# Kernel tuning notes

Hardware: AMD Instinct MI355X
Metric: run time of the kernel (lower is better)

The kernel has to match this reference:

```python
import jax, jax.numpy as jnp
import numpy as np

B, H, W, C = 4, 48, 48, 256
NQ = 8
NH = 8
FFN = 1024


def _dwconv(x, w, b):
    # x: (b,h,w,c); w: (kh,kw,1,c) depthwise; b: (c,)
    p = w.shape[0] // 2
    y = jax.lax.conv_general_dilated(
        x, w, (1, 1), [(p, p), (p, p)],
        dimension_numbers=('NHWC', 'HWIO', 'NHWC'),
        feature_group_count=x.shape[-1])
    return y + b


def _ln(x, g, b, eps=1e-6):
    m = jnp.mean(x, -1, keepdims=True)
    v = jnp.mean((x - m) ** 2, -1, keepdims=True)
    return (x - m) * jax.lax.rsqrt(v + eps) * g + b


def setup_inputs() -> dict:
    key = jax.random.key(0)
    ks = jax.random.split(key, 16)
    s = lambda k, sh, sc=0.02: jax.random.normal(k, sh, jnp.float32) * sc
    return dict(
        x=jax.random.normal(ks[0], (B, H, W, C), jnp.float32),
        queries=jax.random.normal(ks[1], (B, NQ, C), jnp.float32),
        epoch=10,
        pos_w=s(ks[2], (3, 3, 1, C)), pos_b=jnp.zeros((C,), jnp.float32),
        ln1_g=jnp.ones((C,), jnp.float32), ln1_b=jnp.zeros((C,), jnp.float32),
        q_w=s(ks[3], (C, C)), q_b=jnp.zeros((C,), jnp.float32),
        k_w=s(ks[4], (C, C)), k_b=jnp.zeros((C,), jnp.float32),
        v_w=s(ks[5], (C, C)), v_b=jnp.zeros((C,), jnp.float32),
        lepe_w=s(ks[6], (5, 5, 1, C)), lepe_b=jnp.zeros((C,), jnp.float32),
        out_w=s(ks[7], (C, C)), out_b=jnp.zeros((C,), jnp.float32),
        ln2_g=jnp.ones((C,), jnp.float32), ln2_b=jnp.zeros((C,), jnp.float32),
        fc1_w=s(ks[8], (FFN, C)), fc1_b=jnp.zeros((FFN,), jnp.float32),
        fc2_w=s(ks[9], (C, FFN)), fc2_b=jnp.zeros((C,), jnp.float32),
    )


def reference(x, queries, epoch, pos_w, pos_b, ln1_g, ln1_b,
              q_w, q_b, k_w, k_b, v_w, v_b, lepe_w, lepe_b,
              out_w, out_b, ln2_g, ln2_b, fc1_w, fc1_b, fc2_w, fc2_b):
    b, h, w, c = x.shape
    nq = queries.shape[1]
    N = nq + h * w

    # positional DWConv (3x3) residual
    x = x + _dwconv(x, pos_w, pos_b)
    xf = x.reshape(b, h * w, c)
    xq = jnp.concatenate([queries, xf], axis=1)  # (b, N, c)

    # region mask (epoch=10 -> soft softmax phase, tau exp-decayed)
    tau = 2.0 * (0.1 / 2.0) ** (epoch / 200.0)
    logits = jnp.einsum('bnc,bqc->bnq', xf, queries)  # (b, hw, nq)
    p = jax.nn.softmax(logits / tau, axis=-1)
    region = jnp.einsum('bik,bjk->bij', p, p)  # (b, hw, hw)
    mask = jnp.ones((b, N, N), x.dtype).at[:, nq:, nq:].set(region)

    # masked attention (faithful: v_h is built from scaled k, as in source)
    y = _ln(xq, ln1_g, ln1_b)
    q = y @ q_w.T + q_b
    k = y @ k_w.T + k_b
    v = y @ v_w.T + v_b
    lepe = _dwconv(v[:, nq:].reshape(b, h, w, -1), lepe_w, lepe_b).reshape(b, h * w, -1)
    k = k * (c // NH) ** -0.5
    qh = q.reshape(b, N, NH, -1).transpose(0, 2, 1, 3)  # (b, nh, N, d)
    kh = k.reshape(b, N, NH, -1).transpose(0, 2, 1, 3)
    vh = kh  # source assigns v_h from k
    qk = jnp.einsum('bhnd,bhmd->bhnm', qh, kh) * mask[:, None]
    att = jax.nn.softmax(qk, axis=-1)
    o = jnp.einsum('bhnm,bhmd->bhnd', att, vh)
    o = o.transpose(0, 2, 1, 3).reshape(b, N, -1)
    o = o.at[:, nq:, :].add(lepe)
    o = o @ out_w.T + out_b
    xq = xq + o

    # FFN
    z = _ln(xq, ln2_g, ln2_b)
    z = jax.nn.gelu(z @ fc1_w.T + fc1_b, approximate=False)
    z = z @ fc2_w.T + fc2_b
    xq = xq + z

    return xq[:, nq:, :].reshape(b, h, w, c), xq[:, :nq, :]
```

## Files before the change

### kernel.cpp

```cpp
#include <hip/hip_runtime.h>
#include <hip/hip_bf16.h>
#include <math.h>

typedef unsigned short u16;
constexpr int Bc = 4, Hc = 48, Wc = 48, Cc = 256;
constexpr int NQc = 8, HWc = 2304, Nc = 2312, NHc = 8, Dc = 32, FFNc = 1024;
constexpr int MRc = Bc * Nc;
constexpr int KTLDc = 2368;
constexpr float KSCALEc = 0.17677669529663687f;
constexpr float LOG2Ec  = 1.4426950408889634f;

typedef __attribute__((ext_vector_type(8))) short s8v;
typedef __attribute__((ext_vector_type(4))) float f32x4;

__device__ __forceinline__ u16 f2bf(float f) {
    union { __hip_bfloat16 h; u16 u; } c;
    c.h = __float2bfloat16(f);
    return c.u;
}
__device__ __forceinline__ float bf2f(u16 u) {
    return __uint_as_float(((unsigned)u) << 16);
}
__device__ __forceinline__ unsigned cvtpk2(float lo, float hi) {
    unsigned r;
    asm("v_cvt_pk_bf16_f32 %0, %1, %2" : "=v"(r) : "v"(lo), "v"(hi));
    return r;
}
__device__ __forceinline__ float fast_exp2(float x) {
    float r;
    asm("v_exp_f32 %0, %1" : "=v"(r) : "v"(x));
    return r;
}
__device__ __forceinline__ void gload16(const void* g, void* l) {
    __builtin_amdgcn_global_load_lds((const __attribute__((address_space(1))) void*)g,
                                     (__attribute__((address_space(3))) void*)l, 16, 0, 0);
}

__global__ __launch_bounds__(256) void fused_pre_kernel(
    const float* __restrict__ x, const float* __restrict__ queries, const int* __restrict__ epoch,
    const float* __restrict__ pos_w, const float* __restrict__ pos_b,
    const float* __restrict__ ln_g, const float* __restrict__ ln_b,
    const float* __restrict__ qw, const float* __restrict__ kw, const float* __restrict__ vw,
    const float* __restrict__ ow, const float* __restrict__ f1, const float* __restrict__ f2,
    float* __restrict__ xq, u16* __restrict__ ybf, u16* __restrict__ pbf,
    u16* __restrict__ wbf, u16* __restrict__ kt)
{
    int bi = blockIdx.x;
    if (bi >= 9248) {
        int bj = bi - 9248;
        if (bj < 768) {
            int i4 = bj * 256 + threadIdx.x;
            int idx = i4 * 4;
            const float* src; int off;
            if      (idx < 65536)  { src = qw; off = idx; }
            else if (idx < 131072) { src = kw; off = idx - 65536; }
            else if (idx < 196608) { src = vw; off = idx - 131072; }
            else if (idx < 262144) { src = ow; off = idx - 196608; }
            else if (idx < 524288) { src = f1; off = idx - 262144; }
            else                   { src = f2; off = idx - 524288; }
            float4 v = *(const float4*)(src + off);
            ushort4 o;
            o.x = f2bf(v.x); o.y = f2bf(v.y); o.z = f2bf(v.z); o.w = f2bf(v.w);
            *(ushort4*)(wbf + idx) = o;
        } else {
            int idx = (bj - 768) * 256 + threadIdx.x;
            if (idx < 1024 * 56) {
                int row = idx / 56, col = idx - row * 56;
                kt[(size_t)row * KTLDc + 2312 + col] = 0;
            }
        }
        return;
    }
    int blk = bi;
    int b = blk / Nc, n = blk - b * Nc;
    int c = threadIdx.x;
    bool sp = (n >= NQc);
    float val;
    if (sp) {
        int s = n - NQc;
        int hh = s / Wc, ww = s - hh * Wc;
        float acc = pos_b[c];
        float center = x[((b * Hc + hh) * Wc + ww) * Cc + c];
#pragma unroll
        for (int kh = 0; kh < 3; ++kh) {
            int yy = hh + kh - 1;
            if (yy < 0 || yy >= Hc) continue;
#pragma unroll
            for (int kw2 = 0; kw2 < 3; ++kw2) {
                int xx = ww + kw2 - 1;
                if (xx < 0 || xx >= Wc) continue;
                acc += x[((b * Hc + yy) * Wc + xx) * Cc + c] * pos_w[(kh * 3 + kw2) * Cc + c];
            }
        }
        val = center + acc;
    } else {
        val = queries[(b * NQc + n) * Cc + c];
    }
    xq[(size_t)blk * Cc + c] = val;

    float pq[8];
#pragma unroll
    for (int qi = 0; qi < 8; ++qi)
        pq[qi] = sp ? val * queries[(b * NQc + qi) * Cc + c] : 0.f;
    float r0 = val, r1 = val * val;
#pragma unroll
    for (int off = 32; off; off >>= 1) {
        r0 += __shfl_xor(r0, off);
        r1 += __shfl_xor(r1, off);
#pragma unroll
        for (int qi = 0; qi < 8; ++qi) pq[qi] += __shfl_xor(pq[qi], off);
    }
    __shared__ float red[4][10];
    __shared__ float fin[10];
    int wv = c >> 6, ln = c & 63;
    if (ln == 0) {
        red[wv][0] = r0; red[wv][1] = r1;
#pragma unroll
        for (int qi = 0; qi < 8; ++qi) red[wv][2 + qi] = pq[qi];
    }
    __syncthreads();
    if (c < 10) fin[c] = red[0][c] + red[1][c] + red[2][c] + red[3][c];
    __syncthreads();
    float mean = fin[0] * (1.0f / 256.0f);
    float var  = fin[1] * (1.0f / 256.0f) - mean * mean;
    float inv  = rsqrtf(var + 1e-6f);
    ybf[(size_t)blk * Cc + c] = f2bf((val - mean) * inv * ln_g[c] + ln_b[c]);

    if (sp && c < 8) {
        float it = 1.0f / (2.0f * powf(0.05f, (float)(*epoch) / 200.0f));
        float mx = -1e30f;
        float lg[8];
#pragma unroll
        for (int qi = 0; qi < 8; ++qi) { lg[qi] = fin[2 + qi] * it; mx = fmaxf(mx, lg[qi]); }
        float s = 0.f, mine = 0.f;
#pragma unroll
        for (int qi = 0; qi < 8; ++qi) {
            float ev = __expf(lg[qi] - mx);
            s += ev;
            if (qi == c) mine = ev;
        }
        pbf[((size_t)b * HWc + (n - NQc)) * 8 + c] = f2bf(mine / s);
    }
}

__global__ void ln_kernel(const float* __restrict__ in, const float* __restrict__ g,
                          const float* __restrict__ bb, u16* __restrict__ out, int rows)
{
    int gid  = blockIdx.x * blockDim.x + threadIdx.x;
    int wid  = gid >> 6;
    int lane = gid & 63;
    if (wid >= rows) return;
    const float* r = in + (size_t)wid * Cc;
    int c = lane * 4;
    float4 v = *(const float4*)(r + c);
    float s = v.x + v.y + v.z + v.w;
    for (int off = 32; off; off >>= 1) s += __shfl_xor(s, off);
    float mean = s * (1.0f / 256.0f);
    float dx = v.x - mean, dy = v.y - mean, dz = v.z - mean, dw = v.w - mean;
    float ss = dx * dx + dy * dy + dz * dz + dw * dw;
    for (int off = 32; off; off >>= 1) ss += __shfl_xor(ss, off);
    float inv = rsqrtf(ss * (1.0f / 256.0f) + 1e-6f);
    ushort4 o;
    o.x = f2bf(dx * inv * g[c + 0] + bb[c + 0]);
    o.y = f2bf(dy * inv * g[c + 1] + bb[c + 1]);
    o.z = f2bf(dz * inv * g[c + 2] + bb[c + 2]);
    o.w = f2bf(dw * inv * g[c + 3] + bb[c + 3]);
    *(ushort4*)(out + (size_t)wid * Cc + c) = o;
}

template <int ACT, int RESID, int OMODE>
__global__ __launch_bounds__(256) void mfma_gemm_kernel(
    const u16* __restrict__ A, const u16* __restrict__ W,
    const float* __restrict__ bias, const float* resid,
    float* outF, u16* outB,
    int M, int N, int K, float scale)
{
    __shared__ u16 As[128 * 64];
    __shared__ u16 Bs[128 * 64];
    int t = threadIdx.x;
    int w = t >> 6, l = t & 63, lg = l >> 4, lr = l & 15;
    int wm = w >> 1, wn = w & 1;
    int m0 = blockIdx.y * 128, n0 = blockIdx.x * 128;
    f32x4 acc[4][4] = {};
    int lrow = l >> 3, lchunk = (l & 7) * 8;
    for (int k0 = 0; k0 < K; k0 += 64) {
        __syncthreads();
#pragma unroll
        for (int c = 0; c < 4; ++c) {
            int ar = m0 + w * 32 + c * 8 + lrow;
            if (ar >= M) ar = M - 1;
            gload16(A + (size_t)ar * K + k0 + lchunk, As + (w * 32 + c * 8) * 64);
            int br = n0 + w * 32 + c * 8 + lrow;
            gload16(W + (size_t)br * K + k0 + lchunk, Bs + (w * 32 + c * 8) * 64);
        }
        __syncthreads();
#pragma unroll
        for (int kk = 0; kk < 64; kk += 32) {
            s8v aF[4], bF[4];
#pragma unroll
            for (int i = 0; i < 4; ++i)
                aF[i] = *(s8v*)&As[(wm * 64 + i * 16 + lr) * 64 + kk + lg * 8];
#pragma unroll
            for (int j = 0; j < 4; ++j)
                bF[j] = *(s8v*)&Bs[(wn * 64 + j * 16 + lr) * 64 + kk + lg * 8];
#pragma unroll
            for (int i = 0; i < 4; ++i)
#pragma unroll
                for (int j = 0; j < 4; ++j)
                    acc[i][j] = __builtin_amdgcn_mfma_f32_16x16x32_bf16(aF[i], bF[j], acc[i][j], 0, 0, 0);
        }
    }
#pragma unroll
    for (int j = 0; j < 4; ++j) {
        int n = n0 + wn * 64 + j * 16 + lr;
        float bv = bias[n];
#pragma unroll
        for (int i = 0; i < 4; ++i) {
#pragma unroll
            for (int r = 0; r < 4; ++r) {
                int m = m0 + wm * 64 + i * 16 + lg * 4 + r;
                if (m >= M) continue;
                float v = (acc[i][j][r] + bv) * scale;
                if (ACT == 1) {
                    float e = exp2f(2.302118f * (v + 0.044715f * v * v * v));
                    v = v * e * __builtin_amdgcn_rcpf(e + 1.0f);
                }
                if (RESID) v += resid[(size_t)m * N + n];
                if (OMODE == 0) {
                    outF[(size_t)m * N + n] = v;
                } else if (OMODE == 3) {
                    unsigned bb2 = (unsigned)m / 2312u;
                    unsigned tok = (unsigned)m - bb2 * 2312u;
                    size_t ob = (tok >= 8) ? (((size_t)(bb2 * 2304 + tok - 8)) << 8)
                                           : ((size_t)2359296 + (((size_t)(bb2 * 8 + tok)) << 8));
                    outF[ob + n] = v;
                } else {
                    outB[(size_t)m * N + n] = f2bf(v);
                }
            }
        }
    }
}

template <int RESID, int OMODE>
__global__ __launch_bounds__(256) void mfma_gemm64_kernel(
    const u16* __restrict__ A, const u16* __restrict__ W,
    const float* __restrict__ bias, const float* resid,
    float* outF, int M, int N, int K, float scale)
{
    __shared__ u16 As[64 * 64];
    __shared__ u16 Bs[128 * 64];
    int t = threadIdx.x;
    int w = t >> 6, l = t & 63, lg = l >> 4, lr = l & 15;
    int wm = w >> 1, wn = w & 1;
    int m0 = blockIdx.y * 64, n0 = blockIdx.x * 128;
    f32x4 acc[2][4] = {};
    int lrow = l >> 3, lchunk = (l & 7) * 8;
    for (int k0 = 0; k0 < K; k0 += 64) {
        __syncthreads();
#pragma unroll
        for (int c = 0; c < 2; ++c) {
            int ar = m0 + w * 16 + c * 8 + lrow;
            if (ar >= M) ar = M - 1;
            gload16(A + (size_t)ar * K + k0 + lchunk, As + (w * 16 + c * 8) * 64);
        }
#pragma unroll
        for (int c = 0; c < 4; ++c) {
            int br = n0 + w * 32 + c * 8 + lrow;
            gload16(W + (size_t)br * K + k0 + lchunk, Bs + (w * 32 + c * 8) * 64);
        }
        __syncthreads();
#pragma unroll
        for (int kk = 0; kk < 64; kk += 32) {
            s8v aF[2], bF[4];
#pragma unroll
            for (int i = 0; i < 2; ++i)
                aF[i] = *(s8v*)&As[(wm * 32 + i * 16 + lr) * 64 + kk + lg * 8];
#pragma unroll
            for (int j = 0; j < 4; ++j)
                bF[j] = *(s8v*)&Bs[(wn * 64 + j * 16 + lr) * 64 + kk + lg * 8];
#pragma unroll
            for (int i = 0; i < 2; ++i)
#pragma unroll
                for (int j = 0; j < 4; ++j)
                    acc[i][j] = __builtin_amdgcn_mfma_f32_16x16x32_bf16(aF[i], bF[j], acc[i][j], 0, 0, 0);
        }
    }
#pragma unroll
    for (int j = 0; j < 4; ++j) {
        int n = n0 + wn * 64 + j * 16 + lr;
        float bv = bias[n];
#pragma unroll
        for (int i = 0; i < 2; ++i) {
#pragma unroll
            for (int r = 0; r < 4; ++r) {
                int m = m0 + wm * 32 + i * 16 + lg * 4 + r;
                if (m >= M) continue;
                float v = (acc[i][j][r] + bv) * scale;
                if (RESID) v += resid[(size_t)m * N + n];
                if (OMODE == 0) {
                    outF[(size_t)m * N + n] = v;
                } else {
                    unsigned bb2 = (unsigned)m / 2312u;
                    unsigned tok = (unsigned)m - bb2 * 2312u;
                    size_t ob = (tok >= 8) ? (((size_t)(bb2 * 2304 + tok - 8)) << 8)
                                           : ((size_t)2359296 + (((size_t)(bb2 * 8 + tok)) << 8));
                    outF[ob + n] = v;
                }
            }
        }
    }
}

__global__ __launch_bounds__(256) void mfma_gemm_qkv_kernel(
    const u16* __restrict__ A, const u16* __restrict__ W,
    const float* __restrict__ q_b, const float* __restrict__ k_b, const float* __restrict__ v_b,
    u16* __restrict__ outq, u16* __restrict__ outk, u16* __restrict__ outkt, u16* __restrict__ outv)
{
    const int M = MRc, K = Cc;
    __shared__ u16 As[128 * 64];
    __shared__ u16 Bs[128 * 64];
    int t = threadIdx.x;
    int w = t >> 6, l = t & 63, lg = l >> 4, lr = l & 15;
    int wm = w >> 1, wn = w & 1;
    int m0 = blockIdx.y * 128, n0 = blockIdx.x * 128;
    int range = n0 >> 8;
    f32x4 acc[4][4] = {};
    int lrow = l >> 3, lchunk = (l & 7) * 8;
    for (int k0 = 0; k0 < K; k0 += 64) {
        __syncthreads();
#pragma unroll
        for (int c = 0; c < 4; ++c) {
            int ar = m0 + w * 32 + c * 8 + lrow;
            if (ar >= M) ar = M - 1;
            gload16(A + (size_t)ar * K + k0 + lchunk, As + (w * 32 + c * 8) * 64);
            int br = n0 + w * 32 + c * 8 + lrow;
            gload16(W + (size_t)br * K + k0 + lchunk, Bs + (w * 32 + c * 8) * 64);
        }
        __syncthreads();
#pragma unroll
        for (int kk = 0; kk < 64; kk += 32) {
            s8v aF[4], bF[4];
#pragma unroll
            for (int i = 0; i < 4; ++i)
                aF[i] = *(s8v*)&As[(wm * 64 + i * 16 + lr) * 64 + kk + lg * 8];
#pragma unroll
            for (int j = 0; j < 4; ++j)
                bF[j] = *(s8v*)&Bs[(wn * 64 + j * 16 + lr) * 64 + kk + lg * 8];
#pragma unroll
            for (int i = 0; i < 4; ++i)
#pragma unroll
                for (int j = 0; j < 4; ++j)
                    acc[i][j] = __builtin_amdgcn_mfma_f32_16x16x32_bf16(aF[i], bF[j], acc[i][j], 0, 0, 0);
        }
    }
    const float* bias = (range == 0) ? q_b : (range == 1) ? k_b : v_b;
    u16* dst = (range == 0) ? outq : (range == 1) ? outk : outv;
    float scale = (range == 0) ? LOG2Ec : (range == 1) ? KSCALEc : 1.0f;
#pragma unroll
    for (int j = 0; j < 4; ++j) {
        int n = n0 + wn * 64 + j * 16 + lr;
        int nc = n & 255;
        float bv = bias[nc];
#pragma unroll
        for (int i = 0; i < 4; ++i) {
#pragma unroll
            for (int r = 0; r < 4; ++r) {
                int m = m0 + wm * 64 + i * 16 + lg * 4 + r;
                if (m >= M) continue;
                float v = (acc[i][j][r] + bv) * scale;
                u16 hv = f2bf(v);
                dst[(size_t)m * 256 + nc] = hv;
                if (range == 1) {
                    unsigned um = (unsigned)m;
                    unsigned bb = um / 2312u;
                    unsigned nr = um - bb * 2312u;
                    outkt[((size_t)(bb * NHc + (nc >> 5)) * Dc + (nc & 31)) * KTLDc + nr] = hv;
                }
            }
        }
    }
}

__global__ void lepe_conv_add_kernel(const u16* __restrict__ v, const float* __restrict__ w,
                                     const float* __restrict__ bias, u16* __restrict__ o)
{
    int idx = blockIdx.x * 256 + threadIdx.x;
    if (idx >= Bc * HWc * 32) return;
    int cg = (idx & 31) * 8;
    int sp = idx >> 5;
    int ww = sp % Wc;
    int t2 = sp / Wc;
    int hh = t2 % Hc;
    int b  = t2 / Hc;
    float acc[8];
#pragma unroll
    for (int i = 0; i < 8; ++i) acc[i] = bias[cg + i];
#pragma unroll
    for (int kh = 0; kh < 5; ++kh) {
        int yy = hh + kh - 2;
        if (yy < 0 || yy >= Hc) continue;
#pragma unroll
        for (int kw = 0; kw < 5; ++kw) {
            int xx = ww + kw - 2;
            if (xx < 0 || xx >= Wc) continue;
            union { s8v s; u16 u[8]; } uv;
            uv.s = *(const s8v*)&v[((size_t)b * Nc + NQc + yy * Wc + xx) * Cc + cg];
            const float4* wp = (const float4*)&w[(kh * 5 + kw) * Cc + cg];
            float4 w0 = wp[0], w1 = wp[1];
            acc[0] += bf2f(uv.u[0]) * w0.x;
            acc[1] += bf2f(uv.u[1]) * w0.y;
            acc[2] += bf2f(uv.u[2]) * w0.z;
            acc[3] += bf2f(uv.u[3]) * w0.w;
            acc[4] += bf2f(uv.u[4]) * w1.x;
            acc[5] += bf2f(uv.u[5]) * w1.y;
            acc[6] += bf2f(uv.u[6]) * w1.z;
            acc[7] += bf2f(uv.u[7]) * w1.w;
        }
    }
    size_t oi = ((size_t)b * Nc + NQc + hh * Wc + ww) * Cc + cg;
    union { s8v s; u16 u[8]; } ov, res;
    ov.s = *(const s8v*)&o[oi];
#pragma unroll
    for (int i = 0; i < 8; ++i) res.u[i] = f2bf(bf2f(ov.u[i]) + acc[i]);
    *(s8v*)&o[oi] = res.s;
}

__global__ __launch_bounds__(256, 4) void attn_mfma_kernel(const u16* __restrict__ q,
                                                           const u16* __restrict__ k,
                                                           const u16* __restrict__ kt,
                                                           const u16* __restrict__ p,
                                                           u16* __restrict__ o)
{
    constexpr int KT = 64;
    constexpr int NT = (Nc + KT - 1) / KT;
    __shared__ __align__(16) u16 Kls[KT * 40];
    __shared__ __align__(16) u16 Ktls[32 * 88];
    __shared__ __align__(16) unsigned PW[4][16 * 36];

    int flat = blockIdx.x;
    int grp  = flat & 31;
    int qblk = flat >> 5;
    int b = grp >> 3, h = grp & 7;

    int t = threadIdx.x;
    int w = t >> 6, l = t & 63, lg = l >> 4, lr = l & 15;
    int q0 = qblk * 64 + w * 16;

    int qrow = q0 + lr;
    bool qtok = (qrow < NQc);
    int qrc = qrow < Nc ? qrow : Nc - 1;
    s8v qB = *(const s8v*)&q[((size_t)b * Nc + qrc) * Cc + h * Dc + lg * 8];

    s8v pqB = {0, 0, 0, 0, 0, 0, 0, 0};
    if (lg == 0 && qrow >= NQc && qrow < Nc)
        pqB = *(const s8v*)&p[((size_t)b * HWc + (qrow - NQc)) * 8];

    f32x4 accO[2] = {{0.f, 0.f, 0.f, 0.f}, {0.f, 0.f, 0.f, 0.f}};
    float lrun = 0.f;

    int srow = t >> 2, sseg = (t & 3) * 8;
    int td = t >> 3, tks = (t & 7) * 8;
    const u16* ktbase = kt + ((size_t)(b * NHc + h) * Dc + td) * KTLDc;
    const u16* pbase  = p + (size_t)b * HWc * 8;
    unsigned* PWr = &PW[w][lr * 36];
    int bsrc = lg * 20;

    s8v kv8 = {0,0,0,0,0,0,0,0};
    if (srow < Nc)
        kv8 = *(const s8v*)&k[((size_t)b * Nc + srow) * Cc + h * Dc + sseg];
    s8v kt8 = *(const s8v*)&ktbase[tks];

    for (int ti = 0; ti < NT; ++ti) {
        int m0 = ti * KT;
        bool tail = (ti == NT - 1);
        __syncthreads();
        *(s8v*)&Kls[srow * 40 + sseg] = kv8;
        *(s8v*)&Ktls[td * 88 + tks]   = kt8;
        __syncthreads();

        if (ti + 1 < NT) {
            int n0g = m0 + KT;
            kv8 = (s8v){0,0,0,0,0,0,0,0};
            int kvg = n0g + srow;
            if (kvg < Nc)
                kv8 = *(const s8v*)&k[((size_t)b * Nc + kvg) * Cc + h * Dc + sseg];
            kt8 = *(const s8v*)&ktbase[n0g + tks];
        }

        float sc[4][4];
#pragma unroll
        for (int cb = 0; cb < 4; ++cb) {
            s8v kA = *(s8v*)&Kls[(cb * 16 + lr) * 40 + lg * 8];
            f32x4 St = __builtin_amdgcn_mfma_f32_16x16x32_bf16(kA, qB, (f32x4){0.f,0.f,0.f,0.f}, 0, 0, 0);
            s8v pkA = {0, 0, 0, 0, 0, 0, 0, 0};
            if (lg == 0) {
                int kvr = m0 + cb * 16 + lr;
                if (kvr >= NQc && kvr < Nc)
                    pkA = *(const s8v*)&pbase[(size_t)(kvr - NQc) * 8];
            }
            f32x4 Mv = __builtin_amdgcn_mfma_f32_16x16x32_bf16(pkA, pqB, (f32x4){0.f,0.f,0.f,0.f}, 0, 0, 0);
            bool ktok = (ti == 0 && cb == 0 && lg < 2);
#pragma unroll
            for (int j = 0; j < 4; ++j) {
                float mval = (qtok || ktok) ? 1.f : Mv[j];
                sc[cb][j] = St[j] * mval;
            }
        }
        float tsum = 0.f;
#pragma unroll
        for (int cb = 0; cb < 4; ++cb)
#pragma unroll
            for (int j = 0; j < 4; ++j) {
                float ev = fast_exp2(sc[cb][j]);
                if (tail && (cb != 0 || lg >= 2)) ev = 0.f;
                sc[cb][j] = ev;
                tsum += ev;
            }
        tsum += __shfl_xor(tsum, 16);
        tsum += __shfl_xor(tsum, 32);
        lrun += tsum;
#pragma unroll
        for (int cb = 0; cb < 4; ++cb) {
            uint2 pk2;
            pk2.x = cvtpk2(sc[cb][0], sc[cb][1]);
            pk2.y = cvtpk2(sc[cb][2], sc[cb][3]);
            *(uint2*)&PWr[8 * cb + 2 * lg] = pk2;
        }
#pragma unroll
        for (int kc = 0; kc < 2; ++kc) {
            s8v pA = *(s8v*)&PWr[16 * kc + 4 * lg];
#pragma unroll
            for (int db = 0; db < 2; ++db) {
                s8v vB = *(s8v*)&Ktls[(db * 16 + lr) * 88 + kc * 32 + lg * 8];
                accO[db] = __builtin_amdgcn_mfma_f32_16x16x32_bf16(pA, vB, accO[db], 0, 0, 0);
            }
        }
    }

    float lb[4];
#pragma unroll
    for (int j = 0; j < 4; ++j) lb[j] = __shfl(lrun, bsrc + j);
#pragma unroll
    for (int db = 0; db < 2; ++db)
#pragma unroll
        for (int j = 0; j < 4; ++j) {
            int rowg = q0 + lg * 4 + j;
            if (rowg < Nc)
                o[((size_t)b * Nc + rowg) * Cc + h * Dc + db * 16 + lr] = f2bf(accO[db][j] / lb[j]);
        }
}

extern "C" void kernel_launch(void* const* d_in, const int* in_sizes, int n_in,
                              void* d_out, int out_size, void* d_ws, size_t ws_size,
                              hipStream_t stream)
{
    const float* x       = (const float*)d_in[0];
    const float* queries = (const float*)d_in[1];
    const int*   epoch   = (const int*)d_in[2];
    const float* pos_w   = (const float*)d_in[3];
    const float* pos_b   = (const float*)d_in[4];
    const float* ln1_g   = (const float*)d_in[5];
    const float* ln1_b   = (const float*)d_in[6];
    const float* q_w     = (const float*)d_in[7];
    const float* q_b     = (const float*)d_in[8];
    const float* k_w     = (const float*)d_in[9];
    const float* k_b     = (const float*)d_in[10];
    const float* v_w     = (const float*)d_in[11];
    const float* v_b     = (const float*)d_in[12];
    const float* lepe_w  = (const float*)d_in[13];
    const float* lepe_b  = (const float*)d_in[14];
    const float* out_w   = (const float*)d_in[15];
    const float* out_b   = (const float*)d_in[16];
    const float* ln2_g   = (const float*)d_in[17];
    const float* ln2_b   = (const float*)d_in[18];
    const float* fc1_w   = (const float*)d_in[19];
    const float* fc1_b   = (const float*)d_in[20];
    const float* fc2_w   = (const float*)d_in[21];
    const float* fc2_b   = (const float*)d_in[22];

    float* ws = (float*)d_ws;
    float* xq  = ws;
    u16*  ybf  = (u16*)(ws + 2367488);
    u16*  qbf  = (u16*)(ws + 3551232);
    u16*  kbf  = (u16*)(ws + 4734976);
    u16*  ktbf = (u16*)(ws + 5918720);
    u16*  pbf  = (u16*)(ws + 7131136);
    u16*  obf  = (u16*)(ws + 7168000);
    u16*  vbf  = (u16*)(ws + 8351744);
    u16*  wbf  = (u16*)(ws + 9535488);
    u16*  ffn  = qbf;

    u16* w_o  = wbf + 196608;
    u16* w_f1 = wbf + 262144;
    u16* w_f2 = wbf + 524288;

    fused_pre_kernel<<<9248 + 768 + 224, 256, 0, stream>>>(
        x, queries, epoch, pos_w, pos_b, ln1_g, ln1_b,
        q_w, k_w, v_w, out_w, fc1_w, fc2_w,
        xq, ybf, pbf, wbf, ktbf);

    mfma_gemm_qkv_kernel<<<dim3(6, 73), 256, 0, stream>>>(ybf, wbf, q_b, k_b, v_b, qbf, kbf, ktbf, vbf);

    attn_mfma_kernel<<<1184, 256, 0, stream>>>(qbf, kbf, ktbf, pbf, obf);
    lepe_conv_add_kernel<<<1152, 256, 0, stream>>>(vbf, lepe_w, lepe_b, obf);

    mfma_gemm64_kernel<1,0><<<dim3(2, 145), 256, 0, stream>>>(obf, w_o, out_b, xq, xq, MRc, 256, 256, 1.0f);

    ln_kernel<<<2312, 256, 0, stream>>>(xq, ln2_g, ln2_b, ybf, MRc);
    mfma_gemm_kernel<1,0,1><<<dim3(8, 73), 256, 0, stream>>>(ybf, w_f1, fc1_b, nullptr, nullptr, ffn, MRc, 1024, 256, 1.0f);
    mfma_gemm64_kernel<1,3><<<dim3(2, 145), 256, 0, stream>>>(ffn, w_f2, fc2_b, xq, (float*)d_out, MRc, 256, 1024, 1.0f);
}
```

Before: 233.5 us.

## Fuse out-projection GEMM with residual add and LayerNorm2

Replaces the separate output-projection GEMM and LayerNorm kernel with one kernel. Each block computes 32 full rows (all 256 columns), adds bias and residual, writes xq, then reduces row sums across waves in shared memory and emits the bf16 normalized activations. This removes a kernel launch and a full re-read of xq. In exchange the grid has only 289 blocks, and variance is computed as E[x^2]-mean^2, which is less numerically robust.

```diff
diff --git a/kernel.cpp b/kernel.cpp
--- a/kernel.cpp
+++ b/kernel.cpp
@@ -143,31 +143,6 @@
     }
 }
 
-__global__ void ln_kernel(const float* __restrict__ in, const float* __restrict__ g,
-                          const float* __restrict__ bb, u16* __restrict__ out, int rows)
-{
-    int gid  = blockIdx.x * blockDim.x + threadIdx.x;
-    int wid  = gid >> 6;
-    int lane = gid & 63;
-    if (wid >= rows) return;
-    const float* r = in + (size_t)wid * Cc;
-    int c = lane * 4;
-    float4 v = *(const float4*)(r + c);
-    float s = v.x + v.y + v.z + v.w;
-    for (int off = 32; off; off >>= 1) s += __shfl_xor(s, off);
-    float mean = s * (1.0f / 256.0f);
-    float dx = v.x - mean, dy = v.y - mean, dz = v.z - mean, dw = v.w - mean;
-    float ss = dx * dx + dy * dy + dz * dz + dw * dw;
-    for (int off = 32; off; off >>= 1) ss += __shfl_xor(ss, off);
-    float inv = rsqrtf(ss * (1.0f / 256.0f) + 1e-6f);
-    ushort4 o;
-    o.x = f2bf(dx * inv * g[c + 0] + bb[c + 0]);
-    o.y = f2bf(dy * inv * g[c + 1] + bb[c + 1]);
-    o.z = f2bf(dz * inv * g[c + 2] + bb[c + 2]);
-    o.w = f2bf(dw * inv * g[c + 3] + bb[c + 3]);
-    *(ushort4*)(out + (size_t)wid * Cc + c) = o;
-}
-
 template <int ACT, int RESID, int OMODE>
 __global__ __launch_bounds__(256) void mfma_gemm_kernel(
     const u16* __restrict__ A, const u16* __restrict__ W,
@@ -307,6 +282,115 @@
                                            : ((size_t)2359296 + (((size_t)(bb2 * 8 + tok)) << 8));
                     outF[ob + n] = v;
                 }
+            }
+        }
+    }
+}
+
+__global__ __launch_bounds__(256) void mfma_gemm_oln_kernel(
+    const u16* __restrict__ A, const u16* __restrict__ W,
+    const float* __restrict__ bias, float* __restrict__ xq,
+    const float* __restrict__ g, const float* __restrict__ bb,
+    u16* __restrict__ ybf)
+{
+    const int K = Cc;
+    __shared__ u16 As[32 * 64];
+    __shared__ u16 Bs[256 * 64];
+    __shared__ float R[32][4][2];
+    __shared__ float MI[32][2];
+    int t = threadIdx.x;
+    int w = t >> 6, l = t & 63, lg = l >> 4, lr = l & 15;
+    int m0 = blockIdx.x * 32;
+    f32x4 acc[2][4] = {};
+    int lrow = l >> 3, lchunk = (l & 7) * 8;
+    for (int k0 = 0; k0 < K; k0 += 64) {
+        __syncthreads();
+        gload16(A + (size_t)(m0 + w * 8 + lrow) * K + k0 + lchunk, As + (w * 8) * 64);
+#pragma unroll
+        for (int c = 0; c < 8; ++c)
+            gload16(W + (size_t)(w * 64 + c * 8 + lrow) * K + k0 + lchunk, Bs + (w * 64 + c * 8) * 64);
+        __syncthreads();
+#pragma unroll
+        for (int kk = 0; kk < 64; kk += 32) {
+            s8v aF[2], bF[4];
+#pragma unroll
+            for (int i = 0; i < 2; ++i)
+                aF[i] = *(s8v*)&As[(i * 16 + lr) * 64 + kk + lg * 8];
+#pragma unroll
+            for (int j = 0; j < 4; ++j)
+                bF[j] = *(s8v*)&Bs[(w * 64 + j * 16 + lr) * 64 + kk + lg * 8];
+#pragma unroll
+            for (int i = 0; i < 2; ++i)
+#pragma unroll
+                for (int j = 0; j < 4; ++j)
+                    acc[i][j] = __builtin_amdgcn_mfma_f32_16x16x32_bf16(aF[i], bF[j], acc[i][j], 0, 0, 0);
+        }
+    }
+    float s[2][4], ss[2][4];
+#pragma unroll
+    for (int i = 0; i < 2; ++i)
+#pragma unroll
+        for (int r = 0; r < 4; ++r) { s[i][r] = 0.f; ss[i][r] = 0.f; }
+#pragma unroll
+    for (int j = 0; j < 4; ++j) {
+        int n = w * 64 + j * 16 + lr;
+        float bv = bias[n];
+#pragma unroll
+        for (int i = 0; i < 2; ++i) {
+#pragma unroll
+            for (int r = 0; r < 4; ++r) {
+                int m = m0 + i * 16 + lg * 4 + r;
+                float v = acc[i][j][r] + bv + xq[(size_t)m * Cc + n];
+                acc[i][j][r] = v;
+                xq[(size_t)m * Cc + n] = v;
+                s[i][r] += v;
+                ss[i][r] += v * v;
+            }
+        }
+    }
+#pragma unroll
+    for (int i = 0; i < 2; ++i)
+#pragma unroll
+        for (int r = 0; r < 4; ++r) {
+#pragma unroll
+            for (int off = 1; off < 16; off <<= 1) {
+                s[i][r]  += __shfl_xor(s[i][r], off);
+                ss[i][r] += __shfl_xor(ss[i][r], off);
+            }
+        }
+    __syncthreads();
+    if (lr == 0) {
+#pragma unroll
+        for (int i = 0; i < 2; ++i)
+#pragma unroll
+            for (int r = 0; r < 4; ++r) {
+                int row = i * 16 + lg * 4 + r;
+                R[row][w][0] = s[i][r];
+                R[row][w][1] = ss[i][r];
+            }
+    }
+    __syncthreads();
+    if (t < 32) {
+        float tot  = R[t][0][0] + R[t][1][0] + R[t][2][0] + R[t][3][0];
+        float tots = R[t][0][1] + R[t][1][1] + R[t][2][1] + R[t][3][1];
+        float mean = tot * (1.0f / 256.0f);
+        float var  = tots * (1.0f / 256.0f) - mean * mean;
+        MI[t][0] = mean;
+        MI[t][1] = rsqrtf(var + 1e-6f);
+    }
+    __syncthreads();
+#pragma unroll
+    for (int j = 0; j < 4; ++j) {
+        int n = w * 64 + j * 16 + lr;
+        float gv = g[n], bbv = bb[n];
+#pragma unroll
+        for (int i = 0; i < 2; ++i) {
+#pragma unroll
+            for (int r = 0; r < 4; ++r) {
+                int row = i * 16 + lg * 4 + r;
+                float mean = MI[row][0], inv = MI[row][1];
+                int m = m0 + row;
+                ybf[(size_t)m * Cc + n] = f2bf((acc[i][j][r] - mean) * inv * gv + bbv);
             }
         }
     }
@@ -605,9 +689,8 @@
     attn_mfma_kernel<<<1184, 256, 0, stream>>>(qbf, kbf, ktbf, pbf, obf);
     lepe_conv_add_kernel<<<1152, 256, 0, stream>>>(vbf, lepe_w, lepe_b, obf);
 
-    mfma_gemm64_kernel<1,0><<<dim3(2, 145), 256, 0, stream>>>(obf, w_o, out_b, xq, xq, MRc, 256, 256, 1.0f);
-
-    ln_kernel<<<2312, 256, 0, stream>>>(xq, ln2_g, ln2_b, ybf, MRc);
+    mfma_gemm_oln_kernel<<<289, 256, 0, stream>>>(obf, w_o, out_b, xq, ln2_g, ln2_b, ybf);
+
     mfma_gemm_kernel<1,0,1><<<dim3(8, 73), 256, 0, stream>>>(ybf, w_f1, fc1_b, nullptr, nullptr, ffn, MRc, 1024, 256, 1.0f);
     mfma_gemm64_kernel<1,3><<<dim3(2, 145), 256, 0, stream>>>(ffn, w_f2, fc2_b, xq, (float*)d_out, MRc, 256, 1024, 1.0f);
 }
```

Result: faster. 225.8 us (-3.3%).
